# Optimization experiments

Measured on AMD Instinct MI355X. Metric: run time of the kernel, lower is better.

## Reference

```python
import jax, jax.numpy as jnp
import numpy as np

L, E, TOP_K = 3, 8, 2
B, N, D, DS = 256, 1024, 512, 128

def setup_inputs() -> dict:
    key = jax.random.key(0)
    ks = jax.random.split(key, 10)
    s = 0.05  # weight init scale
    return {
        "token": jax.random.normal(ks[0], (B, 1, D), jnp.float32),
        "node_emb": jax.random.normal(ks[1], (B, N, D), jnp.float32),
        "states": jnp.zeros((L, E, B, DS), jnp.float32),
        "Wg": jax.random.normal(ks[2], (L, D, E), jnp.float32) * s,
        "bg": jnp.zeros((L, E), jnp.float32),
        "A": jax.random.normal(ks[3], (L, E, DS), jnp.float32),
        "Bin": jax.random.normal(ks[4], (L, E, D, DS), jnp.float32) * s,
        "Cout": jax.random.normal(ks[5], (L, E, DS, D), jnp.float32) * s,
        "Dsk": jax.random.normal(ks[6], (L, E, D), jnp.float32) * s,
        "Wq": jax.random.normal(ks[7], (D, D), jnp.float32) * s,
        "bq": jnp.zeros((D,), jnp.float32),
    }

def reference(token, node_emb, states, Wg, bg, A, Bin, Cout, Dsk, Wq, bq):
    # token: (B,1,D) -> h: (B,D)
    h = token[:, 0, :]
    lb_loss = jnp.float32(0.0)
    new_states = []
    for l in range(L):
        # --- MoE router: top-k softmax gating ---
        probs = jax.nn.softmax(h @ Wg[l] + bg[l])              # (B,E)
        topv, topi = jax.lax.top_k(probs, TOP_K)               # (B,k)
        gates_k = topv / jnp.sum(topv, axis=-1, keepdims=True)  # renormalized
        oh = jax.nn.one_hot(topi, E, dtype=probs.dtype)        # (B,k,E)
        gate_full = jnp.einsum('bk,bke->be', gates_k, oh)      # (B,E)
        sel = jnp.sum(oh, axis=1) > 0                          # (B,E) bool
        # --- state-space experts (computed densely for all experts) ---
        s = states[l]                                          # (E,B,DS)
        decay = jax.nn.sigmoid(A[l])[:, None, :]               # (E,1,DS)
        s_new = decay * s + jnp.einsum('bd,eds->ebs', h, Bin[l])   # (E,B,DS)
        y = jnp.einsum('ebs,esd->ebd', s_new, Cout[l]) + h[None] * Dsk[l][:, None, :]
        out = jnp.einsum('be,ebd->bd', gate_full, y)           # weighted combine
        # only routed experts advance their state
        keep = sel.T[:, :, None]                               # (E,B,1)
        new_states.append(jnp.where(keep, s_new, s))
        # load-balance loss: E * sum_e mean(probs_e) * mean(frac routed to e)
        lb_loss = lb_loss + E * jnp.sum(jnp.mean(probs, axis=0) * jnp.mean(sel.astype(probs.dtype), axis=0))
        h = h + out                                            # residual
    # --- query projection + logits over nodes ---
    q = h @ Wq + bq                                            # (B,D)
    logits = jnp.einsum('bd,bnd->bn', q, node_emb) / jnp.sqrt(jnp.float32(D))
    return logits, jnp.stack(new_states), lb_loss
```

## Files before the change

kernel.cpp:

```cpp
#include <hip/hip_runtime.h>
#include <math.h>

#define LNUM 3
#define ENUM 8
#define TOPK 2
#define BSZ 256
#define NSZ 1024
#define DSZ 512
#define SSZ 128

typedef float f32x4 __attribute__((ext_vector_type(4)));

template <bool LAST>
__global__ __launch_bounds__(1024) void layer_kernel(
    const float* __restrict__ h_in,
    float* __restrict__ h_out,
    const float* __restrict__ Wg,
    const float* __restrict__ bg,
    const float* __restrict__ A,
    const float* __restrict__ Bin,
    const float* __restrict__ Cout,
    const float* __restrict__ Dsk,
    const float* __restrict__ states,
    float* __restrict__ out_states,
    float* __restrict__ acc_probs,
    float* __restrict__ acc_sel,
    const float* __restrict__ Wq,
    const float* __restrict__ bq,
    float* __restrict__ q_out)
{
    const int b = blockIdx.x;
    const int t = threadIdx.x;
    const int wave = t >> 6;
    const int lane = t & 63;

    __shared__ float h_s[DSZ];
    __shared__ float logit_s[ENUM];
    __shared__ float snew_s[TOPK][SSZ];
    __shared__ float part[1024];

    if (t < DSZ) h_s[t] = h_in[b * DSZ + t];
    __syncthreads();

    if (wave < ENUM) {
        float p = 0.f;
        for (int d = lane; d < DSZ; d += 64) p = fmaf(h_s[d], Wg[d * ENUM + wave], p);
        for (int off = 32; off; off >>= 1) p += __shfl_down(p, off, 64);
        if (lane == 0) logit_s[wave] = p + bg[wave];
    }
    __syncthreads();

    float probs[ENUM];
    float mx = logit_s[0];
    for (int e = 1; e < ENUM; ++e) mx = fmaxf(mx, logit_s[e]);
    float ssum = 0.f;
    for (int e = 0; e < ENUM; ++e) { probs[e] = expf(logit_s[e] - mx); ssum += probs[e]; }
    const float sinv = 1.f / ssum;
    for (int e = 0; e < ENUM; ++e) probs[e] *= sinv;

    int i0 = 0;
    for (int e = 1; e < ENUM; ++e) if (probs[e] > probs[i0]) i0 = e;
    int i1 = -1;
    for (int e = 0; e < ENUM; ++e) {
        if (e == i0) continue;
        if (i1 < 0 || probs[e] > probs[i1]) i1 = e;
    }
    float g0 = probs[i0], g1 = probs[i1];
    const float ginv = 1.f / (g0 + g1);
    g0 *= ginv; g1 *= ginv;

    if (t < ENUM) {
        atomicAdd(&acc_probs[t], probs[t]);
        atomicAdd(&acc_sel[t], (t == i0 || t == i1) ? 1.0f : 0.0f);
    }

    {
        const int k = t >> 9;
        const int r = t & 511;
        const int c = r >> 7;
        const int s = r & 127;
        const int e = k ? i1 : i0;
        const float* Bp = Bin + (size_t)e * DSZ * SSZ + (size_t)(c * 128) * SSZ + s;
        const float* hp = h_s + c * 128;
        float acc = 0.f;
        #pragma unroll 8
        for (int d = 0; d < 128; ++d) acc = fmaf(hp[d], Bp[d * SSZ], acc);
        part[t] = acc;
    }
    __syncthreads();

    if (t < TOPK * SSZ) {
        const int k = t >> 7;
        const int s = t & 127;
        const int e = k ? i1 : i0;
        const int base = k * 512 + s;
        const float sum = part[base] + part[base + 128] + part[base + 256] + part[base + 384];
        const float a = A[e * SSZ + s];
        const float decay = 1.f / (1.f + expf(-a));
        const float sv = states[((size_t)e * BSZ + b) * SSZ + s];
        snew_s[k][s] = decay * sv + sum;
    }
    __syncthreads();

    {
        const int e = t >> 7;
        const int s = t & 127;
        float v;
        if (e == i0)      v = snew_s[0][s];
        else if (e == i1) v = snew_s[1][s];
        else              v = states[((size_t)e * BSZ + b) * SSZ + s];
        out_states[((size_t)e * BSZ + b) * SSZ + s] = v;
    }

    {
        const int half = t >> 9;
        const int d = t & 511;
        const int e = half ? i1 : i0;
        const float* Cp = Cout + (size_t)e * SSZ * DSZ + d;
        const float* sp = snew_s[half];
        float acc = 0.f;
        #pragma unroll 8
        for (int s = 0; s < SSZ; ++s) acc = fmaf(sp[s], Cp[s * DSZ], acc);
        part[t] = acc;
    }
    __syncthreads();

    if (t < DSZ) {
        const float hd = h_s[t];
        const float y0 = part[t]       + hd * Dsk[i0 * DSZ + t];
        const float y1 = part[t + 512] + hd * Dsk[i1 * DSZ + t];
        const float hn = hd + g0 * y0 + g1 * y1;
        if (LAST) h_s[t] = hn;
        else      h_out[b * DSZ + t] = hn;
    }

    if (LAST) {
        __syncthreads();
        {
            const int c = t >> 9;
            const int d = t & 511;
            const float* Wp = Wq + (size_t)(c * 256) * DSZ + d;
            const float* hp = h_s + c * 256;
            float acc = 0.f;
            #pragma unroll 8
            for (int dd = 0; dd < 256; ++dd) acc = fmaf(hp[dd], Wp[dd * DSZ], acc);
            part[t] = acc;
        }
        __syncthreads();
        if (t < DSZ) q_out[b * DSZ + t] = bq[t] + part[t] + part[t + 512];
    }
}

__global__ __launch_bounds__(256) void logits_kernel(
    const float* __restrict__ q, const float* __restrict__ node_emb,
    float* __restrict__ logits,
    const float* __restrict__ acc, float* __restrict__ loss_out)
{
    const int b = blockIdx.y;
    const int wave = threadIdx.x >> 6;
    const int lane = threadIdx.x & 63;

    if (blockIdx.x == 0 && blockIdx.y == 0 && threadIdx.x == 0) {
        float lb = 0.f;
        for (int l = 0; l < LNUM; ++l)
            for (int e = 0; e < ENUM; ++e) {
                const float mp = acc[(l * 2 + 0) * ENUM + e] * (1.0f / BSZ);
                const float ms = acc[(l * 2 + 1) * ENUM + e] * (1.0f / BSZ);
                lb += (float)ENUM * mp * ms;
            }
        loss_out[0] = lb;
    }

    const f32x4* q4 = (const f32x4*)(q + b * DSZ);
    const f32x4 q0 = q4[lane];
    const f32x4 q1 = q4[lane + 64];
    const float scale = 0.04419417382415922f;

    const int n0 = blockIdx.x * 128 + wave * 32;
    #pragma unroll 2
    for (int i = 0; i < 32; ++i) {
        const int n = n0 + i;
        const f32x4* r = (const f32x4*)(node_emb + ((size_t)b * NSZ + n) * DSZ);
        const f32x4 a0 = __builtin_nontemporal_load(&r[lane]);
        const f32x4 a1 = __builtin_nontemporal_load(&r[lane + 64]);
        float dot = a0.x * q0.x + a0.y * q0.y + a0.z * q0.z + a0.w * q0.w
                  + a1.x * q1.x + a1.y * q1.y + a1.z * q1.z + a1.w * q1.w;
        for (int off = 32; off; off >>= 1) dot += __shfl_down(dot, off, 64);
        if (lane == 0) logits[b * NSZ + n] = dot * scale;
    }
}

extern "C" void kernel_launch(void* const* d_in, const int* in_sizes, int n_in,
                              void* d_out, int out_size, void* d_ws, size_t ws_size,
                              hipStream_t stream) {
    const float* token    = (const float*)d_in[0];
    const float* node_emb = (const float*)d_in[1];
    const float* states   = (const float*)d_in[2];
    const float* Wg       = (const float*)d_in[3];
    const float* bg       = (const float*)d_in[4];
    const float* A        = (const float*)d_in[5];
    const float* Bin      = (const float*)d_in[6];
    const float* Cout     = (const float*)d_in[7];
    const float* Dsk      = (const float*)d_in[8];
    const float* Wq       = (const float*)d_in[9];
    const float* bq       = (const float*)d_in[10];

    float* out_logits = (float*)d_out;
    float* out_states = out_logits + (size_t)BSZ * NSZ;
    float* out_loss   = out_states + (size_t)LNUM * ENUM * BSZ * SSZ;

    float* ws_h   = (float*)d_ws;
    float* ws_q   = ws_h + (size_t)BSZ * DSZ;
    float* ws_acc = ws_q + (size_t)BSZ * DSZ;

    (void)hipMemsetAsync(ws_acc, 0, sizeof(float) * LNUM * 2 * ENUM, stream);

    const float* h_cur = token;
    for (int l = 0; l < LNUM; ++l) {
        const bool last = (l == LNUM - 1);
        auto kern = last ? layer_kernel<true> : layer_kernel<false>;
        kern<<<BSZ, 1024, 0, stream>>>(
            h_cur, ws_h,
            Wg  + (size_t)l * DSZ * ENUM,
            bg  + (size_t)l * ENUM,
            A   + (size_t)l * ENUM * SSZ,
            Bin + (size_t)l * ENUM * DSZ * SSZ,
            Cout+ (size_t)l * ENUM * SSZ * DSZ,
            Dsk + (size_t)l * ENUM * DSZ,
            states + (size_t)l * ENUM * BSZ * SSZ,
            out_states + (size_t)l * ENUM * BSZ * SSZ,
            ws_acc + (l * 2 + 0) * ENUM,
            ws_acc + (l * 2 + 1) * ENUM,
            Wq, bq, ws_q);
        h_cur = ws_h;
    }

    dim3 lg(NSZ / 128, BSZ);
    logits_kernel<<<lg, 256, 0, stream>>>(ws_q, node_emb, out_logits, ws_acc, out_loss);
}
```

Baseline: 183.7 us.

## Fuse all three MoE layers and query projection into one kernel with vectorized matvecs

Replaces the three per-layer launches with a single kernel that loops over layers and keeps the hidden vector in shared memory, removing the global h round-trips and two launches. The Bin, Cout and Wq matvecs now use float4 loads with finer d/s chunking and wider partial-sum reductions. The router weights are staged into shared memory first. This raises register pressure and the per-thread vector accumulators, and it keeps one long-running block per batch row.

```diff
diff --git a/kernel.cpp b/kernel.cpp
--- a/kernel.cpp
+++ b/kernel.cpp
@@ -11,143 +11,166 @@
 
 typedef float f32x4 __attribute__((ext_vector_type(4)));
 
-template <bool LAST>
-__global__ __launch_bounds__(1024) void layer_kernel(
-    const float* __restrict__ h_in,
-    float* __restrict__ h_out,
+__global__ __launch_bounds__(1024, 2) void fused_kernel(
+    const float* __restrict__ token,
+    const float* __restrict__ states,
     const float* __restrict__ Wg,
     const float* __restrict__ bg,
     const float* __restrict__ A,
     const float* __restrict__ Bin,
     const float* __restrict__ Cout,
     const float* __restrict__ Dsk,
-    const float* __restrict__ states,
-    float* __restrict__ out_states,
-    float* __restrict__ acc_probs,
-    float* __restrict__ acc_sel,
     const float* __restrict__ Wq,
     const float* __restrict__ bq,
+    float* __restrict__ out_states,
+    float* __restrict__ acc,
     float* __restrict__ q_out)
 {
     const int b = blockIdx.x;
     const int t = threadIdx.x;
     const int wave = t >> 6;
     const int lane = t & 63;
+    const int ehalf = t >> 9;
 
     __shared__ float h_s[DSZ];
+    __shared__ float snew_s[TOPK][SSZ];
     __shared__ float logit_s[ENUM];
-    __shared__ float snew_s[TOPK][SSZ];
-    __shared__ float part[1024];
-
-    if (t < DSZ) h_s[t] = h_in[b * DSZ + t];
+    __shared__ f32x4 part4[1024];
+    float* part = (float*)part4;
+
+    if (t < DSZ) h_s[t] = token[b * DSZ + t];
+
+    for (int l = 0; l < LNUM; ++l) {
+        const float* Wg_l  = Wg  + (size_t)l * DSZ * ENUM;
+        const float* bg_l  = bg  + (size_t)l * ENUM;
+        const float* A_l   = A   + (size_t)l * ENUM * SSZ;
+        const float* Bin_l = Bin + (size_t)l * ENUM * DSZ * SSZ;
+        const float* Cou_l = Cout+ (size_t)l * ENUM * SSZ * DSZ;
+        const float* Dsk_l = Dsk + (size_t)l * ENUM * DSZ;
+        const float* st_l  = states     + (size_t)l * ENUM * BSZ * SSZ;
+        float*       os_l  = out_states + (size_t)l * ENUM * BSZ * SSZ;
+
+        __syncthreads();
+        part4[t] = ((const f32x4*)Wg_l)[t];
+        __syncthreads();
+
+        if (wave < ENUM) {
+            float p = 0.f;
+            #pragma unroll
+            for (int i = 0; i < 8; ++i) {
+                const int d = lane + i * 64;
+                p = fmaf(h_s[d], part[d * ENUM + wave], p);
+            }
+            for (int off = 32; off; off >>= 1) p += __shfl_down(p, off, 64);
+            if (lane == 0) logit_s[wave] = p + bg_l[wave];
+        }
+        __syncthreads();
+
+        float probs[ENUM];
+        float mx = logit_s[0];
+        for (int e = 1; e < ENUM; ++e) mx = fmaxf(mx, logit_s[e]);
+        float ssum = 0.f;
+        for (int e = 0; e < ENUM; ++e) { probs[e] = expf(logit_s[e] - mx); ssum += probs[e]; }
+        const float sinv = 1.f / ssum;
+        for (int e = 0; e < ENUM; ++e) probs[e] *= sinv;
+
+        int i0 = 0;
+        for (int e = 1; e < ENUM; ++e) if (probs[e] > probs[i0]) i0 = e;
+        int i1 = -1;
+        for (int e = 0; e < ENUM; ++e) {
+            if (e == i0) continue;
+            if (i1 < 0 || probs[e] > probs[i1]) i1 = e;
+        }
+        float g0 = probs[i0], g1 = probs[i1];
+        const float ginv = 1.f / (g0 + g1);
+        g0 *= ginv; g1 *= ginv;
+
+        if (t < ENUM) {
+            atomicAdd(&acc[(l * 2 + 0) * ENUM + t], probs[t]);
+            atomicAdd(&acc[(l * 2 + 1) * ENUM + t], (t == i0 || t == i1) ? 1.0f : 0.0f);
+        }
+        const int esel = ehalf ? i1 : i0;
+
+        {
+            const int rem   = t & 511;
+            const int c     = rem >> 5;
+            const int squad = rem & 31;
+            const float* Bp = Bin_l + (size_t)esel * DSZ * SSZ;
+            const int d0 = c * 32;
+            f32x4 acc4 = {0.f, 0.f, 0.f, 0.f};
+            #pragma unroll
+            for (int d = 0; d < 32; ++d)
+                acc4 += *(const f32x4*)(Bp + (size_t)(d0 + d) * SSZ + squad * 4) * h_s[d0 + d];
+            part4[(ehalf * 16 + c) * 32 + squad] = acc4;
+        }
+        __syncthreads();
+
+        if (t < TOPK * SSZ) {
+            const int k = t >> 7, s = t & 127;
+            const int e = k ? i1 : i0;
+            float sum = 0.f;
+            #pragma unroll
+            for (int c = 0; c < 16; ++c) sum += part[(k * 16 + c) * 128 + s];
+            const float a = A_l[e * SSZ + s];
+            const float decay = 1.f / (1.f + expf(-a));
+            snew_s[k][s] = decay * st_l[((size_t)e * BSZ + b) * SSZ + s] + sum;
+        }
+        __syncthreads();
+
+        {
+            const int e = t >> 7, s = t & 127;
+            float v;
+            if (e == i0)      v = snew_s[0][s];
+            else if (e == i1) v = snew_s[1][s];
+            else              v = st_l[((size_t)e * BSZ + b) * SSZ + s];
+            os_l[((size_t)e * BSZ + b) * SSZ + s] = v;
+        }
+
+        {
+            const int rem   = t & 511;
+            const int chunk = rem >> 7;
+            const int dquad = rem & 127;
+            const float* Cp = Cou_l + (size_t)esel * SSZ * DSZ;
+            const float* sp = snew_s[ehalf];
+            const int s0 = chunk * 32;
+            f32x4 acc4 = {0.f, 0.f, 0.f, 0.f};
+            #pragma unroll
+            for (int s = 0; s < 32; ++s)
+                acc4 += *(const f32x4*)(Cp + (size_t)(s0 + s) * DSZ + dquad * 4) * sp[s0 + s];
+            part4[(ehalf * 4 + chunk) * 128 + dquad] = acc4;
+        }
+        __syncthreads();
+
+        if (t < DSZ) {
+            const float hd = h_s[t];
+            float y0 = hd * Dsk_l[i0 * DSZ + t];
+            float y1 = hd * Dsk_l[i1 * DSZ + t];
+            #pragma unroll
+            for (int c = 0; c < 4; ++c) {
+                y0 += part[c * 512 + t];
+                y1 += part[(4 + c) * 512 + t];
+            }
+            h_s[t] = hd + g0 * y0 + g1 * y1;
+        }
+    }
+
     __syncthreads();
-
-    if (wave < ENUM) {
-        float p = 0.f;
-        for (int d = lane; d < DSZ; d += 64) p = fmaf(h_s[d], Wg[d * ENUM + wave], p);
-        for (int off = 32; off; off >>= 1) p += __shfl_down(p, off, 64);
-        if (lane == 0) logit_s[wave] = p + bg[wave];
+    {
+        const int chunk = t >> 7;
+        const int dquad = t & 127;
+        const int dd0 = chunk * 64;
+        f32x4 acc4 = {0.f, 0.f, 0.f, 0.f};
+        #pragma unroll 8
+        for (int i = 0; i < 64; ++i)
+            acc4 += *(const f32x4*)(Wq + (size_t)(dd0 + i) * DSZ + dquad * 4) * h_s[dd0 + i];
+        part4[chunk * 128 + dquad] = acc4;
     }
     __syncthreads();
-
-    float probs[ENUM];
-    float mx = logit_s[0];
-    for (int e = 1; e < ENUM; ++e) mx = fmaxf(mx, logit_s[e]);
-    float ssum = 0.f;
-    for (int e = 0; e < ENUM; ++e) { probs[e] = expf(logit_s[e] - mx); ssum += probs[e]; }
-    const float sinv = 1.f / ssum;
-    for (int e = 0; e < ENUM; ++e) probs[e] *= sinv;
-
-    int i0 = 0;
-    for (int e = 1; e < ENUM; ++e) if (probs[e] > probs[i0]) i0 = e;
-    int i1 = -1;
-    for (int e = 0; e < ENUM; ++e) {
-        if (e == i0) continue;
-        if (i1 < 0 || probs[e] > probs[i1]) i1 = e;
-    }
-    float g0 = probs[i0], g1 = probs[i1];
-    const float ginv = 1.f / (g0 + g1);
-    g0 *= ginv; g1 *= ginv;
-
-    if (t < ENUM) {
-        atomicAdd(&acc_probs[t], probs[t]);
-        atomicAdd(&acc_sel[t], (t == i0 || t == i1) ? 1.0f : 0.0f);
-    }
-
-    {
-        const int k = t >> 9;
-        const int r = t & 511;
-        const int c = r >> 7;
-        const int s = r & 127;
-        const int e = k ? i1 : i0;
-        const float* Bp = Bin + (size_t)e * DSZ * SSZ + (size_t)(c * 128) * SSZ + s;
-        const float* hp = h_s + c * 128;
-        float acc = 0.f;
-        #pragma unroll 8
-        for (int d = 0; d < 128; ++d) acc = fmaf(hp[d], Bp[d * SSZ], acc);
-        part[t] = acc;
-    }
-    __syncthreads();
-
-    if (t < TOPK * SSZ) {
-        const int k = t >> 7;
-        const int s = t & 127;
-        const int e = k ? i1 : i0;
-        const int base = k * 512 + s;
-        const float sum = part[base] + part[base + 128] + part[base + 256] + part[base + 384];
-        const float a = A[e * SSZ + s];
-        const float decay = 1.f / (1.f + expf(-a));
-        const float sv = states[((size_t)e * BSZ + b) * SSZ + s];
-        snew_s[k][s] = decay * sv + sum;
-    }
-    __syncthreads();
-
-    {
-        const int e = t >> 7;
-        const int s = t & 127;
-        float v;
-        if (e == i0)      v = snew_s[0][s];
-        else if (e == i1) v = snew_s[1][s];
-        else              v = states[((size_t)e * BSZ + b) * SSZ + s];
-        out_states[((size_t)e * BSZ + b) * SSZ + s] = v;
-    }
-
-    {
-        const int half = t >> 9;
-        const int d = t & 511;
-        const int e = half ? i1 : i0;
-        const float* Cp = Cout + (size_t)e * SSZ * DSZ + d;
-        const float* sp = snew_s[half];
-        float acc = 0.f;
-        #pragma unroll 8
-        for (int s = 0; s < SSZ; ++s) acc = fmaf(sp[s], Cp[s * DSZ], acc);
-        part[t] = acc;
-    }
-    __syncthreads();
-
     if (t < DSZ) {
-        const float hd = h_s[t];
-        const float y0 = part[t]       + hd * Dsk[i0 * DSZ + t];
-        const float y1 = part[t + 512] + hd * Dsk[i1 * DSZ + t];
-        const float hn = hd + g0 * y0 + g1 * y1;
-        if (LAST) h_s[t] = hn;
-        else      h_out[b * DSZ + t] = hn;
-    }
-
-    if (LAST) {
-        __syncthreads();
-        {
-            const int c = t >> 9;
-            const int d = t & 511;
-            const float* Wp = Wq + (size_t)(c * 256) * DSZ + d;
-            const float* hp = h_s + c * 256;
-            float acc = 0.f;
-            #pragma unroll 8
-            for (int dd = 0; dd < 256; ++dd) acc = fmaf(hp[dd], Wp[dd * DSZ], acc);
-            part[t] = acc;
-        }
-        __syncthreads();
-        if (t < DSZ) q_out[b * DSZ + t] = bq[t] + part[t] + part[t + 512];
+        float qv = bq[t];
+        #pragma unroll
+        for (int c = 0; c < 8; ++c) qv += part[c * 512 + t];
+        q_out[b * DSZ + t] = qv;
     }
 }
 
@@ -209,31 +232,14 @@
     float* out_states = out_logits + (size_t)BSZ * NSZ;
     float* out_loss   = out_states + (size_t)LNUM * ENUM * BSZ * SSZ;
 
-    float* ws_h   = (float*)d_ws;
-    float* ws_q   = ws_h + (size_t)BSZ * DSZ;
+    float* ws_q   = (float*)d_ws;
     float* ws_acc = ws_q + (size_t)BSZ * DSZ;
 
     (void)hipMemsetAsync(ws_acc, 0, sizeof(float) * LNUM * 2 * ENUM, stream);
 
-    const float* h_cur = token;
-    for (int l = 0; l < LNUM; ++l) {
-        const bool last = (l == LNUM - 1);
-        auto kern = last ? layer_kernel<true> : layer_kernel<false>;
-        kern<<<BSZ, 1024, 0, stream>>>(
-            h_cur, ws_h,
-            Wg  + (size_t)l * DSZ * ENUM,
-            bg  + (size_t)l * ENUM,
-            A   + (size_t)l * ENUM * SSZ,
-            Bin + (size_t)l * ENUM * DSZ * SSZ,
-            Cout+ (size_t)l * ENUM * SSZ * DSZ,
-            Dsk + (size_t)l * ENUM * DSZ,
-            states + (size_t)l * ENUM * BSZ * SSZ,
-            out_states + (size_t)l * ENUM * BSZ * SSZ,
-            ws_acc + (l * 2 + 0) * ENUM,
-            ws_acc + (l * 2 + 1) * ENUM,
-            Wq, bq, ws_q);
-        h_cur = ws_h;
-    }
+    fused_kernel<<<BSZ, 1024, 0, stream>>>(
+        token, states, Wg, bg, A, Bin, Cout, Dsk, Wq, bq,
+        out_states, ws_acc, ws_q);
 
     dim3 lg(NSZ / 128, BSZ);
     logits_kernel<<<lg, 256, 0, stream>>>(ws_q, node_emb, out_logits, ws_acc, out_loss);
```

Measured after the change: 172.5 us. -6.1%, faster.
